# Performance work log

Measured on AMD Instinct MI355X. Metric: run time of the kernel, lower is better.

Reference implementation:

```python
import jax, jax.numpy as jnp
import numpy as np

IMG_W, IMG_H = 960.0, 512.0          # NETWORK.IMAGE_SIZE
HM_W, HM_H = 240.0, 128.0            # NETWORK.HEATMAP_SIZE (w, h)
GRID_SIZE = (8000.0, 8000.0, 2000.0)
CUBE = (80, 80, 20)
SPACE_CENTER = (0.0, -500.0, 800.0)


def _make_grid():
    # compute_grid: meshgrid(indexing='ij'), flattened to [nbins, 3]
    gx = np.linspace(-GRID_SIZE[0] / 2, GRID_SIZE[0] / 2, CUBE[0]) + SPACE_CENTER[0]
    gy = np.linspace(-GRID_SIZE[1] / 2, GRID_SIZE[1] / 2, CUBE[1]) + SPACE_CENTER[1]
    gz = np.linspace(-GRID_SIZE[2] / 2, GRID_SIZE[2] / 2, CUBE[2]) + SPACE_CENTER[2]
    X, Y, Z = np.meshgrid(gx, gy, gz, indexing='ij')
    return jnp.asarray(np.stack([X.ravel(), Y.ravel(), Z.ravel()], 1), jnp.float32)


def setup_inputs() -> dict:
    key = jax.random.key(0)
    ks = jax.random.split(key, 8)
    n, B, J, H, W = 5, 4, 15, 128, 240
    heatmaps = jax.random.uniform(ks[0], (n, B, J, H, W), jnp.float32)
    # cameras: rotate about z per view, positioned so all grid points have depth > 0
    thetas = np.linspace(0.0, 2 * np.pi, n, endpoint=False)
    Rs = np.zeros((n, B, 3, 3), np.float32)
    for v, th in enumerate(thetas):
        c, s = np.cos(th), np.sin(th)
        Rs[v, :] = np.array([[c, -s, 0.0], [s, c, 0.0], [0.0, 0.0, 1.0]], np.float32)
    cam_R = jnp.asarray(Rs)
    cam_T = jnp.asarray(np.tile(np.array([0.0, 0.0, -5000.0], np.float32), (n, B, 1))) \
        + 50.0 * jax.random.normal(ks[1], (n, B, 3), jnp.float32)
    cam_f = 1500.0 + 20.0 * jax.random.normal(ks[2], (n, B, 2), jnp.float32)
    cam_c = jnp.asarray([IMG_W / 2, IMG_H / 2], jnp.float32) \
        + 5.0 * jax.random.normal(ks[3], (n, B, 2), jnp.float32)
    cam_k = jnp.asarray(np.tile(np.array([-0.01, 0.001, 0.0], np.float32), (n, B, 1))) \
        + 1e-4 * jax.random.normal(ks[4], (n, B, 3), jnp.float32)
    cam_p = 1e-3 * jax.random.normal(ks[5], (n, B, 2), jnp.float32)
    center = jnp.asarray([IMG_W / 2, IMG_H / 2], jnp.float32) \
        + 10.0 * jax.random.normal(ks[6], (n, B, 2), jnp.float32)
    scale = jnp.asarray([IMG_W / 200.0, IMG_H / 200.0], jnp.float32) \
        * (1.0 + 0.05 * jax.random.uniform(ks[7], (n, B, 2), jnp.float32))
    return {"heatmaps": heatmaps, "cam_R": cam_R, "cam_T": cam_T, "cam_f": cam_f,
            "cam_c": cam_c, "cam_k": cam_k, "cam_p": cam_p, "center": center,
            "scale": scale}


def _forward(heatmaps, cam_R, cam_T, cam_f, cam_c, cam_k, cam_p, center, scale):
    n, B, J, Hd, Wd = heatmaps.shape
    grid = _make_grid()                                   # [N, 3]
    N = grid.shape[0]
    # --- project_pose (pinhole + radial/tangential distortion) ---
    diff = grid[None, None] - cam_T[:, :, None, :]        # [v,b,N,3]
    xcam = jnp.einsum('vbij,vbnj->vbni', cam_R, diff)     # [v,b,N,3]
    y = xcam[..., :2] / (xcam[..., 2:3] + 1e-5)
    r2 = jnp.sum(y * y, -1)                               # [v,b,N]
    radial = 1.0 + cam_k[..., 0:1] * r2 + cam_k[..., 1:2] * r2 ** 2 + cam_k[..., 2:3] * r2 ** 3
    tan = cam_p[..., 0:1] * y[..., 1] + cam_p[..., 1:2] * y[..., 0]
    y = y * (radial + 2.0 * tan)[..., None] \
        + jnp.stack([cam_p[..., 1], cam_p[..., 0]], -1)[:, :, None, :] * r2[..., None]
    pix = cam_f[:, :, None, :] * y + cam_c[:, :, None, :]  # [v,b,N,2]
    # --- bounding: inside image of size (width, height) = 2*center ---
    wh = 2.0 * center                                      # [v,b,2]
    bounding = ((pix[..., 0] >= 0) & (pix[..., 1] >= 0)
                & (pix[..., 0] < wh[..., 0:1]) & (pix[..., 1] < wh[..., 1:2])
                ).astype(heatmaps.dtype)                   # [v,b,N]
    maxwh = jnp.maximum(wh[..., 0], wh[..., 1])[..., None, None]
    pix = jnp.clip(pix, -1.0, maxwh)
    # --- get_transform(center, scale, 0, img_size) + do_transform ---
    hs = 200.0 * scale                                     # [v,b,2]
    img = jnp.asarray([IMG_W, IMG_H], heatmaps.dtype)
    t_scale = img / hs                                     # diag of affine
    t_off = img * (-center / hs + 0.5)
    xy = pix * t_scale[:, :, None, :] + t_off[:, :, None, :]
    # scale to heatmap resolution, then to normalized [-1,1] (align_corners=True)
    xy = xy * (jnp.asarray([HM_W, HM_H], heatmaps.dtype) / img)
    sg = xy / jnp.asarray([HM_W - 1, HM_H - 1], heatmaps.dtype) * 2.0 - 1.0
    sg = jnp.clip(sg, -1.1, 1.1)
    # --- bilinear grid_sample, align_corners=True, zeros padding ---
    px = (sg[..., 0] + 1.0) * 0.5 * (Wd - 1)
    py = (sg[..., 1] + 1.0) * 0.5 * (Hd - 1)
    x0 = jnp.floor(px)
    y0 = jnp.floor(py)
    wx = px - x0
    wy = py - y0
    x0i = x0.astype(jnp.int32)
    y0i = y0.astype(jnp.int32)
    flat = heatmaps.reshape(n, B, J, Hd * Wd)

    def corner(xi, yi):
        valid = ((xi >= 0) & (xi < Wd) & (yi >= 0) & (yi < Hd)).astype(heatmaps.dtype)
        idx = jnp.clip(yi, 0, Hd - 1) * Wd + jnp.clip(xi, 0, Wd - 1)   # [v,b,N]
        g = jnp.take_along_axis(flat, idx[:, :, None, :], axis=3)       # [v,b,J,N]
        return g * valid[:, :, None, :]

    val = (corner(x0i, y0i) * ((1 - wx) * (1 - wy))[:, :, None, :]
           + corner(x0i + 1, y0i) * (wx * (1 - wy))[:, :, None, :]
           + corner(x0i, y0i + 1) * ((1 - wx) * wy)[:, :, None, :]
           + corner(x0i + 1, y0i + 1) * (wx * wy)[:, :, None, :])       # [v,b,J,N]
    # --- per-view cube = bounding * sampled; combine over views ---
    cubes_v = bounding[:, :, None, :] * val
    num = jnp.sum(cubes_v * bounding[:, :, None, :], axis=0)            # [b,J,N]
    den = jnp.sum(bounding, axis=0)[:, None, :] + 1e-6
    cubes = jnp.clip(num / den, 0.0, 1.0).reshape(B, J, CUBE[0], CUBE[1], CUBE[2])
    grids = jnp.broadcast_to(grid, (B, N, 3))
    return cubes, grids


def reference(heatmaps, cam_R, cam_T, cam_f, cam_c, cam_k, cam_p, center, scale):
    return _forward(heatmaps, cam_R, cam_T, cam_f, cam_c, cam_k, cam_p, center, scale)
```

## Files before the change

### kernel.cpp

```cpp
#include <hip/hip_runtime.h>
#include <hip/hip_fp16.h>

#define NV 5
#define NB 4
#define NJ 15
#define HD 128
#define WD 240
#define CX 80
#define CY 80
#define CZ 20
#define NPTS (CX*CY*CZ)
#define JP16 16
#define BLOCKS_PER_B (NPTS/256)
#define NWG (NB*BLOCKS_PER_B)

struct ViewSample {
    float w[4];
    int   cx0, cx1, cy0, cy1;
    float bnd;
};

__device__ __forceinline__ ViewSample project_one_view(
    float gx, float gy, float gz,
    const float* __restrict__ cam_R, const float* __restrict__ cam_T,
    const float* __restrict__ cam_f, const float* __restrict__ cam_c,
    const float* __restrict__ cam_k, const float* __restrict__ cam_p,
    const float* __restrict__ center, const float* __restrict__ scale,
    int cb)
{
    const float* R = cam_R + cb*9;
    const float* T = cam_T + cb*3;
    float fx = cam_f[cb*2+0], fy = cam_f[cb*2+1];
    float ccx = cam_c[cb*2+0], ccy = cam_c[cb*2+1];
    float k0 = cam_k[cb*3+0], k1 = cam_k[cb*3+1], k2 = cam_k[cb*3+2];
    float p0 = cam_p[cb*2+0], p1 = cam_p[cb*2+1];
    float cenx = center[cb*2+0], ceny = center[cb*2+1];
    float scx = scale[cb*2+0],  scy = scale[cb*2+1];

    float dx = gx - T[0], dy = gy - T[1], dz = gz - T[2];
    float xc = R[0]*dx + R[1]*dy + R[2]*dz;
    float yc = R[3]*dx + R[4]*dy + R[5]*dz;
    float zc = R[6]*dx + R[7]*dy + R[8]*dz;
    float invz = 1.0f / (zc + 1e-5f);
    float ux = xc * invz, uy = yc * invz;
    float r2 = ux*ux + uy*uy;
    float radial = 1.0f + k0*r2 + k1*(r2*r2) + k2*(r2*r2*r2);
    float tn = p0*uy + p1*ux;
    float m  = radial + 2.0f*tn;
    float xd = ux*m + p1*r2;
    float yd = uy*m + p0*r2;
    float pixx = fx*xd + ccx;
    float pixy = fy*yd + ccy;

    float whx = 2.0f*cenx, why = 2.0f*ceny;
    float bnd = (pixx >= 0.0f && pixy >= 0.0f && pixx < whx && pixy < why) ? 1.0f : 0.0f;
    float mwh = fmaxf(whx, why);
    pixx = fminf(fmaxf(pixx, -1.0f), mwh);
    pixy = fminf(fmaxf(pixy, -1.0f), mwh);

    float hsx = 200.0f*scx, hsy = 200.0f*scy;
    float xyx = (pixx * (960.0f/hsx) + 960.0f*(-cenx/hsx + 0.5f)) * 0.25f;
    float xyy = (pixy * (512.0f/hsy) + 512.0f*(-ceny/hsy + 0.5f)) * 0.25f;
    float sgx = (xyx / 239.0f) * 2.0f - 1.0f;
    float sgy = (xyy / 127.0f) * 2.0f - 1.0f;
    sgx = fminf(fmaxf(sgx, -1.1f), 1.1f);
    sgy = fminf(fmaxf(sgy, -1.1f), 1.1f);

    float pxf = (sgx + 1.0f) * 0.5f * 239.0f;
    float pyf = (sgy + 1.0f) * 0.5f * 127.0f;
    float x0f = floorf(pxf), y0f = floorf(pyf);
    float wx = pxf - x0f, wy = pyf - y0f;
    int x0 = (int)x0f, y0 = (int)y0f;
    int x1 = x0 + 1,   y1 = y0 + 1;
    float vx0 = (x0 >= 0 && x0 < WD) ? 1.0f : 0.0f;
    float vx1 = (x1 >= 0 && x1 < WD) ? 1.0f : 0.0f;
    float vy0 = (y0 >= 0 && y0 < HD) ? 1.0f : 0.0f;
    float vy1 = (y1 >= 0 && y1 < HD) ? 1.0f : 0.0f;

    ViewSample s;
    s.cx0 = min(max(x0, 0), WD-1);
    s.cx1 = min(max(x1, 0), WD-1);
    s.cy0 = min(max(y0, 0), HD-1);
    s.cy1 = min(max(y1, 0), HD-1);
    s.w[0] = (1.0f-wx)*(1.0f-wy) * vx0*vy0 * bnd;
    s.w[1] = wx*(1.0f-wy)        * vx1*vy0 * bnd;
    s.w[2] = (1.0f-wx)*wy        * vx0*vy1 * bnd;
    s.w[3] = wx*wy               * vx1*vy1 * bnd;
    s.bnd = bnd;
    return s;
}

__device__ __forceinline__ void grid_coords(int nn, float& gx, float& gy, float& gz) {
    int iz = nn % CZ;
    int iy = (nn / CZ) % CY;
    int ix = nn / (CZ*CY);
    gx = (float)(((double)ix * (8000.0/79.0) - 4000.0) + 0.0);
    gy = (float)(((double)iy * (8000.0/79.0) - 4000.0) - 500.0);
    gz = (float)(((double)iz * (2000.0/19.0) - 1000.0) + 800.0);
}

__global__ __launch_bounds__(256) void hm_transpose_f16x4(
    const float* __restrict__ hm, __half* __restrict__ out)
{
    int idx = blockIdx.x * 256 + threadIdx.x;
    if (idx >= NV*NB*HD*(WD/4)) return;
    int xq = idx % (WD/4);
    int y  = (idx / (WD/4)) % HD;
    int vb = idx / ((WD/4)*HD);
    const float* src = hm + ((size_t)vb*NJ*HD + (size_t)y)*WD + xq*4;

    float4 ld[NJ];
    #pragma unroll
    for (int j = 0; j < NJ; ++j)
        ld[j] = *reinterpret_cast<const float4*>(src + (size_t)j*HD*WD);

    union { float4 f4[8]; __half h[64]; } u;
    #pragma unroll
    for (int j = 0; j < NJ; ++j) {
        u.h[0*JP16 + j] = __float2half(ld[j].x);
        u.h[1*JP16 + j] = __float2half(ld[j].y);
        u.h[2*JP16 + j] = __float2half(ld[j].z);
        u.h[3*JP16 + j] = __float2half(ld[j].w);
    }
    u.h[0*JP16 + 15] = __float2half(0.0f);
    u.h[1*JP16 + 15] = __float2half(0.0f);
    u.h[2*JP16 + 15] = __float2half(0.0f);
    u.h[3*JP16 + 15] = __float2half(0.0f);

    float4* dst = reinterpret_cast<float4*>(out + (size_t)idx * 64);
    #pragma unroll
    for (int q = 0; q < 8; ++q) dst[q] = u.f4[q];
}

__global__ __launch_bounds__(256) void project_kernel_f16(
    const __half* __restrict__ hmT,
    const float* __restrict__ cam_R, const float* __restrict__ cam_T,
    const float* __restrict__ cam_f, const float* __restrict__ cam_c,
    const float* __restrict__ cam_k, const float* __restrict__ cam_p,
    const float* __restrict__ center, const float* __restrict__ scale,
    float* __restrict__ out_cubes, float* __restrict__ out_grids)
{
    int wg   = (int)blockIdx.x;
    int swz  = (wg % 8) * (NWG/8) + wg / 8;
    const int b  = swz / BLOCKS_PER_B;
    const int nn = (swz % BLOCKS_PER_B)*256 + threadIdx.x;

    float gx, gy, gz;
    grid_coords(nn, gx, gy, gz);

    float acc[NJ];
    #pragma unroll
    for (int j = 0; j < NJ; ++j) acc[j] = 0.0f;
    float den = 0.0f;

    #pragma unroll 1
    for (int v = 0; v < NV; ++v) {
        int cb = v*NB + b;
        ViewSample s = project_one_view(gx, gy, gz, cam_R, cam_T, cam_f, cam_c,
                                        cam_k, cam_p, center, scale, cb);
        den += s.bnd;
        float wsum = s.w[0] + s.w[1] + s.w[2] + s.w[3];
        if (__any(wsum > 0.0f)) {
            int base = cb * (HD*WD*JP16);
            int off[4];
            off[0] = base + (s.cy0*WD + s.cx0)*JP16;
            off[1] = base + (s.cy0*WD + s.cx1)*JP16;
            off[2] = base + (s.cy1*WD + s.cx0)*JP16;
            off[3] = base + (s.cy1*WD + s.cx1)*JP16;
            #pragma unroll
            for (int c = 0; c < 4; ++c) {
                float w = s.w[c];
                if (w != 0.0f) {
                    union { float4 f4[2]; __half2 h2[8]; } u;
                    const float4* p = reinterpret_cast<const float4*>(hmT + off[c]);
                    u.f4[0] = p[0];
                    u.f4[1] = p[1];
                    #pragma unroll
                    for (int k = 0; k < 7; ++k) {
                        float2 f = __half22float2(u.h2[k]);
                        acc[2*k]   += w * f.x;
                        acc[2*k+1] += w * f.y;
                    }
                    float2 f7 = __half22float2(u.h2[7]);
                    acc[14] += w * f7.x;
                }
            }
        }
    }

    float inv_den = 1.0f / (den + 1e-6f);
    #pragma unroll
    for (int j = 0; j < NJ; ++j) {
        float val = fminf(fmaxf(acc[j]*inv_den, 0.0f), 1.0f);
        out_cubes[((size_t)b*NJ + j)*NPTS + nn] = val;
    }
    float* g = out_grids + ((size_t)b*NPTS + nn)*3;
    g[0] = gx; g[1] = gy; g[2] = gz;
}

__global__ __launch_bounds__(256) void project_kernel_direct(
    const float* __restrict__ hm,
    const float* __restrict__ cam_R, const float* __restrict__ cam_T,
    const float* __restrict__ cam_f, const float* __restrict__ cam_c,
    const float* __restrict__ cam_k, const float* __restrict__ cam_p,
    const float* __restrict__ center, const float* __restrict__ scale,
    float* __restrict__ out_cubes, float* __restrict__ out_grids)
{
    const int b  = blockIdx.x / BLOCKS_PER_B;
    const int nn = (blockIdx.x % BLOCKS_PER_B)*256 + threadIdx.x;

    float gx, gy, gz;
    grid_coords(nn, gx, gy, gz);

    float acc[NJ];
    #pragma unroll
    for (int j = 0; j < NJ; ++j) acc[j] = 0.0f;
    float den = 0.0f;

    #pragma unroll 1
    for (int v = 0; v < NV; ++v) {
        int cb = v*NB + b;
        ViewSample s = project_one_view(gx, gy, gz, cam_R, cam_T, cam_f, cam_c,
                                        cam_k, cam_p, center, scale, cb);
        den += s.bnd;
        float wsum = s.w[0] + s.w[1] + s.w[2] + s.w[3];
        if (__any(wsum > 0.0f)) {
            int off[4];
            off[0] = s.cy0*WD + s.cx0;
            off[1] = s.cy0*WD + s.cx1;
            off[2] = s.cy1*WD + s.cx0;
            off[3] = s.cy1*WD + s.cx1;
            #pragma unroll
            for (int j = 0; j < NJ; ++j) {
                const float* base = hm + ((size_t)cb*NJ + j)*(HD*WD);
                acc[j] += s.w[0]*base[off[0]] + s.w[1]*base[off[1]]
                        + s.w[2]*base[off[2]] + s.w[3]*base[off[3]];
            }
        }
    }

    float inv_den = 1.0f / (den + 1e-6f);
    #pragma unroll
    for (int j = 0; j < NJ; ++j) {
        float val = fminf(fmaxf(acc[j]*inv_den, 0.0f), 1.0f);
        out_cubes[((size_t)b*NJ + j)*NPTS + nn] = val;
    }
    float* g = out_grids + ((size_t)b*NPTS + nn)*3;
    g[0] = gx; g[1] = gy; g[2] = gz;
}

extern "C" void kernel_launch(void* const* d_in, const int* in_sizes, int n_in,
                              void* d_out, int out_size, void* d_ws, size_t ws_size,
                              hipStream_t stream) {
    const float* hm     = (const float*)d_in[0];
    const float* cam_R  = (const float*)d_in[1];
    const float* cam_T  = (const float*)d_in[2];
    const float* cam_f  = (const float*)d_in[3];
    const float* cam_c  = (const float*)d_in[4];
    const float* cam_k  = (const float*)d_in[5];
    const float* cam_p  = (const float*)d_in[6];
    const float* center = (const float*)d_in[7];
    const float* scale  = (const float*)d_in[8];

    float* out_cubes = (float*)d_out;
    float* out_grids = out_cubes + (size_t)NB*NJ*NPTS;

    size_t need = (size_t)NV*NB*HD*WD*JP16*sizeof(__half);
    if (ws_size >= need) {
        __half* hmT = (__half*)d_ws;
        hipLaunchKernelGGL(hm_transpose_f16x4,
                           dim3((NV*NB*HD*(WD/4))/256), dim3(256), 0, stream, hm, hmT);
        hipLaunchKernelGGL(project_kernel_f16,
                           dim3(NWG), dim3(256), 0, stream,
                           hmT, cam_R, cam_T, cam_f, cam_c, cam_k, cam_p,
                           center, scale, out_cubes, out_grids);
    } else {
        hipLaunchKernelGGL(project_kernel_direct,
                           dim3(NWG), dim3(256), 0, stream,
                           hm, cam_R, cam_T, cam_f, cam_c, cam_k, cam_p,
                           center, scale, out_cubes, out_grids);
    }
}
```

Measured before the change: 129.6 us.

## Split views across wavefronts and reduce per-point sums through LDS

The main projection kernel now gives each of five wavefronts one camera view for a 64-point chunk, instead of having one thread loop over all five views. Each wave writes its partial per-joint sums and bounding value to shared memory. After a barrier, four waves combine the partials and write the cubes while a sixth wave writes the grid coordinates. This is meant to raise parallelism and hide gather latency, at the cost of LDS traffic, a barrier, and three idle waves in a 512-thread block. Per-lane skipping of zero-weight gathers is also added, in both the split kernel and the fallback kernel.

After: 131.9 us. No clear change (+1.7%).

```diff
diff --git a/kernel.cpp b/kernel.cpp
--- a/kernel.cpp
+++ b/kernel.cpp
@@ -11,8 +11,9 @@
 #define CZ 20
 #define NPTS (CX*CY*CZ)
 #define JP16 16
-#define BLOCKS_PER_B (NPTS/256)
-#define NWG (NB*BLOCKS_PER_B)
+#define PTS_PER_BLK 64
+#define CHUNKS (NPTS/PTS_PER_BLK)
+#define NWG2 (NB*CHUNKS)
 
 struct ViewSample {
     float w[4];
@@ -132,7 +133,7 @@
     for (int q = 0; q < 8; ++q) dst[q] = u.f4[q];
 }
 
-__global__ __launch_bounds__(256) void project_kernel_f16(
+__global__ __launch_bounds__(512) void project_kernel_split(
     const __half* __restrict__ hmT,
     const float* __restrict__ cam_R, const float* __restrict__ cam_T,
     const float* __restrict__ cam_f, const float* __restrict__ cam_c,
@@ -140,37 +141,43 @@
     const float* __restrict__ center, const float* __restrict__ scale,
     float* __restrict__ out_cubes, float* __restrict__ out_grids)
 {
-    int wg   = (int)blockIdx.x;
-    int swz  = (wg % 8) * (NWG/8) + wg / 8;
-    const int b  = swz / BLOCKS_PER_B;
-    const int nn = (swz % BLOCKS_PER_B)*256 + threadIdx.x;
+    __shared__ float lds_acc[NJ][NV][PTS_PER_BLK];
+    __shared__ float lds_den[NV][PTS_PER_BLK];
+
+    int wg  = (int)blockIdx.x;
+    int swz = (wg % 8) * (NWG2/8) + wg / 8;
+    const int b     = swz / CHUNKS;
+    const int chunk = swz % CHUNKS;
+    const int n0    = chunk * PTS_PER_BLK;
+
+    const int w    = threadIdx.x >> 6;
+    const int lane = threadIdx.x & 63;
+    const int nn   = n0 + lane;
 
     float gx, gy, gz;
     grid_coords(nn, gx, gy, gz);
 
-    float acc[NJ];
-    #pragma unroll
-    for (int j = 0; j < NJ; ++j) acc[j] = 0.0f;
-    float den = 0.0f;
-
-    #pragma unroll 1
-    for (int v = 0; v < NV; ++v) {
-        int cb = v*NB + b;
+    if (w < NV) {
+        const int v  = w;
+        const int cb = v*NB + b;
         ViewSample s = project_one_view(gx, gy, gz, cam_R, cam_T, cam_f, cam_c,
                                         cam_k, cam_p, center, scale, cb);
-        den += s.bnd;
+        float acc[NJ];
+        #pragma unroll
+        for (int j = 0; j < NJ; ++j) acc[j] = 0.0f;
+
         float wsum = s.w[0] + s.w[1] + s.w[2] + s.w[3];
         if (__any(wsum > 0.0f)) {
-            int base = cb * (HD*WD*JP16);
-            int off[4];
-            off[0] = base + (s.cy0*WD + s.cx0)*JP16;
-            off[1] = base + (s.cy0*WD + s.cx1)*JP16;
-            off[2] = base + (s.cy1*WD + s.cx0)*JP16;
-            off[3] = base + (s.cy1*WD + s.cx1)*JP16;
-            #pragma unroll
-            for (int c = 0; c < 4; ++c) {
-                float w = s.w[c];
-                if (w != 0.0f) {
+            if (wsum > 0.0f) {
+                int base = cb * (HD*WD*JP16);
+                int off[4];
+                off[0] = base + (s.cy0*WD + s.cx0)*JP16;
+                off[1] = base + (s.cy0*WD + s.cx1)*JP16;
+                off[2] = base + (s.cy1*WD + s.cx0)*JP16;
+                off[3] = base + (s.cy1*WD + s.cx1)*JP16;
+                #pragma unroll
+                for (int c = 0; c < 4; ++c) {
+                    float wc = s.w[c];
                     union { float4 f4[2]; __half2 h2[8]; } u;
                     const float4* p = reinterpret_cast<const float4*>(hmT + off[c]);
                     u.f4[0] = p[0];
@@ -178,24 +185,38 @@
                     #pragma unroll
                     for (int k = 0; k < 7; ++k) {
                         float2 f = __half22float2(u.h2[k]);
-                        acc[2*k]   += w * f.x;
-                        acc[2*k+1] += w * f.y;
+                        acc[2*k]   += wc * f.x;
+                        acc[2*k+1] += wc * f.y;
                     }
                     float2 f7 = __half22float2(u.h2[7]);
-                    acc[14] += w * f7.x;
+                    acc[14] += wc * f7.x;
                 }
             }
         }
-    }
-
-    float inv_den = 1.0f / (den + 1e-6f);
-    #pragma unroll
-    for (int j = 0; j < NJ; ++j) {
-        float val = fminf(fmaxf(acc[j]*inv_den, 0.0f), 1.0f);
-        out_cubes[((size_t)b*NJ + j)*NPTS + nn] = val;
-    }
-    float* g = out_grids + ((size_t)b*NPTS + nn)*3;
-    g[0] = gx; g[1] = gy; g[2] = gz;
+        #pragma unroll
+        for (int j = 0; j < NJ; ++j) lds_acc[j][v][lane] = acc[j];
+        lds_den[v][lane] = s.bnd;
+    }
+
+    __syncthreads();
+
+    if (w < 4) {
+        float den = lds_den[0][lane] + lds_den[1][lane] + lds_den[2][lane]
+                  + lds_den[3][lane] + lds_den[4][lane];
+        float inv = 1.0f / (den + 1e-6f);
+        int j0 = w*4;
+        int j1 = (w == 3) ? NJ : j0 + 4;
+        for (int j = j0; j < j1; ++j) {
+            float sv = lds_acc[j][0][lane] + lds_acc[j][1][lane]
+                     + lds_acc[j][2][lane] + lds_acc[j][3][lane]
+                     + lds_acc[j][4][lane];
+            float val = fminf(fmaxf(sv * inv, 0.0f), 1.0f);
+            out_cubes[((size_t)b*NJ + j)*NPTS + nn] = val;
+        }
+    } else if (w == 5) {
+        float* g = out_grids + ((size_t)b*NPTS + nn)*3;
+        g[0] = gx; g[1] = gy; g[2] = gz;
+    }
 }
 
 __global__ __launch_bounds__(256) void project_kernel_direct(
@@ -206,8 +227,8 @@
     const float* __restrict__ center, const float* __restrict__ scale,
     float* __restrict__ out_cubes, float* __restrict__ out_grids)
 {
-    const int b  = blockIdx.x / BLOCKS_PER_B;
-    const int nn = (blockIdx.x % BLOCKS_PER_B)*256 + threadIdx.x;
+    const int b  = blockIdx.x / (NPTS/256);
+    const int nn = (blockIdx.x % (NPTS/256))*256 + threadIdx.x;
 
     float gx, gy, gz;
     grid_coords(nn, gx, gy, gz);
@@ -224,17 +245,17 @@
                                         cam_k, cam_p, center, scale, cb);
         den += s.bnd;
         float wsum = s.w[0] + s.w[1] + s.w[2] + s.w[3];
-        if (__any(wsum > 0.0f)) {
-            int off[4];
-            off[0] = s.cy0*WD + s.cx0;
-            off[1] = s.cy0*WD + s.cx1;
-            off[2] = s.cy1*WD + s.cx0;
-            off[3] = s.cy1*WD + s.cx1;
+        if (__any(wsum > 0.0f) && wsum > 0.0f) {
+            int o00 = s.cy0*WD + s.cx0;
+            int o10 = s.cy0*WD + s.cx1;
+            int o01 = s.cy1*WD + s.cx0;
+            int o11 = s.cy1*WD + s.cx1;
+            const float* base = hm + (size_t)cb*NJ*(HD*WD);
             #pragma unroll
             for (int j = 0; j < NJ; ++j) {
-                const float* base = hm + ((size_t)cb*NJ + j)*(HD*WD);
-                acc[j] += s.w[0]*base[off[0]] + s.w[1]*base[off[1]]
-                        + s.w[2]*base[off[2]] + s.w[3]*base[off[3]];
+                const float* p = base + (size_t)j*(HD*WD);
+                acc[j] += s.w[0]*p[o00] + s.w[1]*p[o10]
+                        + s.w[2]*p[o01] + s.w[3]*p[o11];
             }
         }
     }
@@ -270,13 +291,13 @@
         __half* hmT = (__half*)d_ws;
         hipLaunchKernelGGL(hm_transpose_f16x4,
                            dim3((NV*NB*HD*(WD/4))/256), dim3(256), 0, stream, hm, hmT);
-        hipLaunchKernelGGL(project_kernel_f16,
-                           dim3(NWG), dim3(256), 0, stream,
+        hipLaunchKernelGGL(project_kernel_split,
+                           dim3(NWG2), dim3(512), 0, stream,
                            hmT, cam_R, cam_T, cam_f, cam_c, cam_k, cam_p,
                            center, scale, out_cubes, out_grids);
     } else {
         hipLaunchKernelGGL(project_kernel_direct,
-                           dim3(NWG), dim3(256), 0, stream,
+                           dim3(NB*(NPTS/256)), dim3(256), 0, stream,
                            hm, cam_R, cam_T, cam_f, cam_c, cam_k, cam_p,
                            center, scale, out_cubes, out_grids);
     }
```
